# Kernel optimization log

Measured on AMD Instinct MI355X. Metric: run time of the kernel, lower is better.

The kernel has to match this reference:

```python
import jax, jax.numpy as jnp
import numpy as np

B, T, D = 2, 2048, 512
HEADS, DIM_HEAD, MAX_LAG = 8, 64, 5
INNER = HEADS * DIM_HEAD


def setup_inputs() -> dict:
    key = jax.random.key(0)
    k0, k1, k2, k3, k4 = jax.random.split(key, 5)
    x = jax.random.normal(k0, (B, T, D), dtype=jnp.float32)
    # Linear weights stored as (in, out); torch applies x @ W.T with W (out, in).
    Wq = jax.random.normal(k1, (D, INNER), dtype=jnp.float32) * (1.0 / np.sqrt(D))
    Wk = jax.random.normal(k2, (D, INNER), dtype=jnp.float32) * (1.0 / np.sqrt(D))
    Wv = jax.random.normal(k3, (D, INNER), dtype=jnp.float32) * (1.0 / np.sqrt(D))
    Wo = jax.random.normal(k4, (INNER, D), dtype=jnp.float32) * (1.0 / np.sqrt(INNER))
    bo = jnp.zeros((D,), dtype=jnp.float32)
    # Module's init: lag_weights = log(exp(-lags/(max_lag/3))) = -lags/(max_lag/3)
    lags = jnp.arange(MAX_LAG + 1, dtype=jnp.float32)
    lag_weights = jnp.broadcast_to(-(lags / (MAX_LAG / 3.0)), (HEADS, MAX_LAG + 1)).astype(jnp.float32)
    return {"x": x, "Wq": Wq, "Wk": Wk, "Wv": Wv, "Wo": Wo, "bo": bo, "lag_weights": lag_weights}


def reference(x, Wq, Wk, Wv, Wo, bo, lag_weights):
    b, t, _ = x.shape
    h, dh = HEADS, DIM_HEAD
    scale = dh ** -0.5
    # context defaults to x (self-attention)
    q = (x @ Wq).reshape(b, t, h, dh).transpose(0, 2, 1, 3)  # b h t d
    k = (x @ Wk).reshape(b, t, h, dh).transpose(0, 2, 1, 3)
    v = (x @ Wv).reshape(b, t, h, dh).transpose(0, 2, 1, 3)
    sim = jnp.einsum('bhid,bhjd->bhij', q, k) * scale  # b h t t
    # causal mask: keep j <= i
    causal = jnp.tril(jnp.ones((t, t), dtype=bool))
    neg = -jnp.finfo(sim.dtype).max
    sim = jnp.where(causal[None, None], sim, neg)
    # learned additive time-lag bias: lag_adj[h,i,j] = softmax(lag_weights)[h, clamp(i-j,0,MAX_LAG)]
    ti = jnp.arange(t)
    time_lags = jnp.clip(ti[:, None] - ti[None, :], 0, MAX_LAG)  # t t
    lag_probs = jax.nn.softmax(lag_weights, axis=-1)  # h (L+1)
    lag_adj = lag_probs[:, time_lags]  # h t t
    sim = sim + lag_adj[None]
    attn = jax.nn.softmax(sim, axis=-1)
    out = jnp.einsum('bhij,bhjd->bhid', attn, v)
    out = out.transpose(0, 2, 1, 3).reshape(b, t, h * dh)  # b t inner
    return out @ Wo + bo  # dropout is identity at eval
```

## Files before the change

kernel.cpp:

```cpp
#include <hip/hip_runtime.h>
#include <hip/hip_bf16.h>

#define BB 2
#define TT 2048
#define DD 512
#define HH 8
#define DH 64
#define INNER 512
#define MAXLAG 5

typedef __attribute__((ext_vector_type(8))) short short8;
typedef __attribute__((ext_vector_type(4))) float floatx4;
typedef unsigned short ushort_t;

__device__ inline unsigned short f2bf(float f) {
    unsigned u = __float_as_uint(f);
    unsigned r = (u + 0x7FFFu + ((u >> 16) & 1u)) >> 16;
    return (unsigned short)r;
}
__device__ inline float bf2f(unsigned short u) {
    return __uint_as_float(((unsigned)u) << 16);
}

__device__ __forceinline__ void gload16(ushort_t* lds, const ushort_t* g) {
    __builtin_amdgcn_global_load_lds(
        (const __attribute__((address_space(1))) void*)g,
        (__attribute__((address_space(3))) void*)lds, 16, 0, 0);
}

__global__ __launch_bounds__(256)
void cvt_kernel(const float* __restrict__ x,
                const float* __restrict__ wq, const float* __restrict__ wk,
                const float* __restrict__ wv, const float* __restrict__ wo,
                ushort_t* __restrict__ xb,
                ushort_t* __restrict__ wqkvt, ushort_t* __restrict__ wot)
{
    __shared__ float T[32][33];
    const int bid = blockIdx.x;
    if (bid < 1024) {
        int off = (bid * 256 + threadIdx.x) * 8;
        float4 a = *(const float4*)&x[off];
        float4 b = *(const float4*)&x[off + 4];
        ushort_t t[8];
        t[0] = f2bf(a.x); t[1] = f2bf(a.y); t[2] = f2bf(a.z); t[3] = f2bf(a.w);
        t[4] = f2bf(b.x); t[5] = f2bf(b.y); t[6] = f2bf(b.z); t[7] = f2bf(b.w);
        *(uint4*)&xb[off] = *(const uint4*)t;
        return;
    }
    const int r = bid - 1024;
    const int z = r >> 8;
    const int tile = r & 255;
    const float* s = (z == 0) ? wq : (z == 1) ? wk : (z == 2) ? wv : wo;
    ushort_t*    d = (z < 3) ? (wqkvt + (size_t)z * 512 * 512) : wot;
    const int k0 = (tile & 15) * 32;
    const int n0 = (tile >> 4) * 32;
    {
        const int kk = threadIdx.x >> 3;
        const int n4 = (threadIdx.x & 7) * 4;
        float4 v = *(const float4*)&s[(size_t)(k0 + kk) * 512 + n0 + n4];
        T[kk][n4 + 0] = v.x; T[kk][n4 + 1] = v.y;
        T[kk][n4 + 2] = v.z; T[kk][n4 + 3] = v.w;
    }
    __syncthreads();
    {
        const int nn = threadIdx.x >> 3;
        const int k4 = (threadIdx.x & 7) * 4;
        ushort4 o;
        o.x = f2bf(T[k4 + 0][nn]); o.y = f2bf(T[k4 + 1][nn]);
        o.z = f2bf(T[k4 + 2][nn]); o.w = f2bf(T[k4 + 3][nn]);
        *(ushort4*)&d[(size_t)(n0 + nn) * 512 + k0 + k4] = o;
    }
}

#define QM 128
#define QN 64
#define QKS 64

__global__ __launch_bounds__(256)
void gemm_qkv(const ushort_t* __restrict__ A, const ushort_t* __restrict__ Bw,
              ushort_t* __restrict__ q, ushort_t* __restrict__ k,
              ushort_t* __restrict__ vt)
{
    __shared__ ushort_t As[QM * QKS];
    __shared__ ushort_t Bs[QN * QKS];

    const int tid  = threadIdx.x;
    const int wave = tid >> 6;
    const int lane = tid & 63;
    const int quad = lane >> 4;
    const int l15  = lane & 15;
    const int wr   = wave >> 1;
    const int wc   = wave & 1;
    const int bm   = blockIdx.y * QM;
    const int bn   = blockIdx.x * QN;

    const int lr = lane >> 3;
    const int lc = lane & 7;

    const ushort_t* ap[4];
#pragma unroll
    for (int j = 0; j < 4; ++j) {
        const int row = wave * 32 + j * 8 + lr;
        const int c   = (lc - row) & 7;
        ap[j] = &A[(size_t)(bm + row) * DD + c * 8];
    }
    const ushort_t* bp[2];
#pragma unroll
    for (int j = 0; j < 2; ++j) {
        const int row = wave * 16 + j * 8 + lr;
        const int c   = (lc - row) & 7;
        bp[j] = &Bw[(size_t)(bn + row) * DD + c * 8];
    }
    ushort_t* lA0 = &As[(size_t)(wave * 256 +   0) * 8];
    ushort_t* lA1 = &As[(size_t)(wave * 256 +  64) * 8];
    ushort_t* lA2 = &As[(size_t)(wave * 256 + 128) * 8];
    ushort_t* lA3 = &As[(size_t)(wave * 256 + 192) * 8];
    ushort_t* lB0 = &Bs[(size_t)(wave * 128 +  0) * 8];
    ushort_t* lB1 = &Bs[(size_t)(wave * 128 + 64) * 8];

    floatx4 acc[4][2];
#pragma unroll
    for (int i = 0; i < 4; ++i)
#pragma unroll
        for (int j = 0; j < 2; ++j) acc[i][j] = (floatx4){0.f, 0.f, 0.f, 0.f};

#pragma unroll
    for (int k0 = 0; k0 < DD; k0 += QKS) {
        __syncthreads();
        gload16(lA0, ap[0] + k0);
        gload16(lA1, ap[1] + k0);
        gload16(lA2, ap[2] + k0);
        gload16(lA3, ap[3] + k0);
        gload16(lB0, bp[0] + k0);
        gload16(lB1, bp[1] + k0);
        __syncthreads();

#pragma unroll
        for (int kk = 0; kk < 2; ++kk) {
            short8 af[4], bfr[2];
#pragma unroll
            for (int mt = 0; mt < 4; ++mt) {
                const int row = wr * 64 + mt * 16 + l15;
                af[mt] = *(const short8*)
                    &As[((row << 3) + ((kk * 4 + quad + row) & 7)) * 8];
            }
#pragma unroll
            for (int nt = 0; nt < 2; ++nt) {
                const int row = wc * 32 + nt * 16 + l15;
                bfr[nt] = *(const short8*)
                    &Bs[((row << 3) + ((kk * 4 + quad + row) & 7)) * 8];
            }
#pragma unroll
            for (int mt = 0; mt < 4; ++mt)
#pragma unroll
                for (int nt = 0; nt < 2; ++nt)
                    acc[mt][nt] = __builtin_amdgcn_mfma_f32_16x16x32_bf16(
                        af[mt], bfr[nt], acc[mt][nt], 0, 0, 0);
        }
    }

    const int z = bn >> 9;
    if (z == 2) {
#pragma unroll
        for (int mt = 0; mt < 4; ++mt) {
            const int m0 = bm + wr * 64 + mt * 16 + quad * 4;
            const int b  = m0 >> 11;
            const int t0 = m0 & 2047;
#pragma unroll
            for (int nt = 0; nt < 2; ++nt) {
                const int n  = bn + wc * 32 + nt * 16 + l15 - 1024;
                const int h  = n >> 6, dd = n & 63;
                ushort4 o;
                o.x = f2bf(acc[mt][nt][0]); o.y = f2bf(acc[mt][nt][1]);
                o.z = f2bf(acc[mt][nt][2]); o.w = f2bf(acc[mt][nt][3]);
                *(ushort4*)&vt[((size_t)((b * 8 + h) * 64 + dd)) * 2048 + t0] = o;
            }
        }
        return;
    }
    ushort_t* O = (z == 0) ? q : k;
    const int nb = bn - z * 512;
#pragma unroll
    for (int mt = 0; mt < 4; ++mt) {
#pragma unroll
        for (int nt = 0; nt < 2; ++nt) {
            const int n = nb + wc * 32 + nt * 16 + l15;
#pragma unroll
            for (int reg = 0; reg < 4; ++reg) {
                const int m = bm + wr * 64 + mt * 16 + quad * 4 + reg;
                O[(size_t)m * 512 + n] = f2bf(acc[mt][nt][reg]);
            }
        }
    }
}

__global__ __launch_bounds__(256)
void gemm_proj(const ushort_t* __restrict__ A, const ushort_t* __restrict__ Bw,
               float* __restrict__ O, const float* __restrict__ bias)
{
    __shared__ ushort_t As[64 * 64];
    __shared__ ushort_t Bs[64 * 64];

    const int tid  = threadIdx.x;
    const int wave = tid >> 6;
    const int lane = tid & 63;
    const int quad = lane >> 4;
    const int l15  = lane & 15;
    const int wr   = wave >> 1;
    const int wc   = wave & 1;
    const int bm   = blockIdx.y * 64;
    const int bn   = blockIdx.x * 64;

    const int lr = lane >> 3;
    const int lc = lane & 7;

    const ushort_t* ap[2];
    const ushort_t* bp[2];
#pragma unroll
    for (int j = 0; j < 2; ++j) {
        const int row = wave * 16 + j * 8 + lr;
        const int c   = (lc - row) & 7;
        ap[j] = &A[(size_t)(bm + row) * INNER + c * 8];
        bp[j] = &Bw[(size_t)(bn + row) * INNER + c * 8];
    }
    ushort_t* lA0 = &As[(size_t)(wave * 128 +  0) * 8];
    ushort_t* lA1 = &As[(size_t)(wave * 128 + 64) * 8];
    ushort_t* lB0 = &Bs[(size_t)(wave * 128 +  0) * 8];
    ushort_t* lB1 = &Bs[(size_t)(wave * 128 + 64) * 8];

    floatx4 acc[2][2];
#pragma unroll
    for (int i = 0; i < 2; ++i)
#pragma unroll
        for (int j = 0; j < 2; ++j) acc[i][j] = (floatx4){0.f, 0.f, 0.f, 0.f};

#pragma unroll
    for (int k0 = 0; k0 < INNER; k0 += 64) {
        __syncthreads();
        gload16(lA0, ap[0] + k0);
        gload16(lA1, ap[1] + k0);
        gload16(lB0, bp[0] + k0);
        gload16(lB1, bp[1] + k0);
        __syncthreads();

#pragma unroll
        for (int kk = 0; kk < 2; ++kk) {
            short8 af[2], bfr[2];
#pragma unroll
            for (int mt = 0; mt < 2; ++mt) {
                const int row = wr * 32 + mt * 16 + l15;
                af[mt] = *(const short8*)
                    &As[((row << 3) + ((kk * 4 + quad + row) & 7)) * 8];
            }
#pragma unroll
            for (int nt = 0; nt < 2; ++nt) {
                const int row = wc * 32 + nt * 16 + l15;
                bfr[nt] = *(const short8*)
                    &Bs[((row << 3) + ((kk * 4 + quad + row) & 7)) * 8];
            }
#pragma unroll
            for (int mt = 0; mt < 2; ++mt)
#pragma unroll
                for (int nt = 0; nt < 2; ++nt)
                    acc[mt][nt] = __builtin_amdgcn_mfma_f32_16x16x32_bf16(
                        af[mt], bfr[nt], acc[mt][nt], 0, 0, 0);
        }
    }

    float bv[2];
#pragma unroll
    for (int nt = 0; nt < 2; ++nt)
        bv[nt] = bias[bn + wc * 32 + nt * 16 + l15];
#pragma unroll
    for (int mt = 0; mt < 2; ++mt) {
#pragma unroll
        for (int nt = 0; nt < 2; ++nt) {
            const int n = bn + wc * 32 + nt * 16 + l15;
#pragma unroll
            for (int reg = 0; reg < 4; ++reg) {
                const int m = bm + wr * 32 + mt * 16 + quad * 4 + reg;
                O[(size_t)m * 512 + n] = acc[mt][nt][reg] + bv[nt];
            }
        }
    }
}

#define PAD 72
#define MFIX 10.0f

__global__ __launch_bounds__(256)
void attn_mfma(const ushort_t* __restrict__ Qg,
               const ushort_t* __restrict__ Kg,
               const ushort_t* __restrict__ Vtg,
               const float* __restrict__ lagw,
               ushort_t* __restrict__ Opart,
               float* __restrict__ Lpart,
               ushort_t* __restrict__ ao)
{
    __shared__ ushort_t Ks[64 * 8 * 8];
    __shared__ ushort_t Vts[64 * 8 * 8];
    __shared__ ushort_t Pl[4][16][PAD];

    const int tid  = threadIdx.x;
    const int wave = tid >> 6;
    const int lane = tid & 63;
    const int quad = lane >> 4;
    const int l15  = lane & 15;

    const int f  = blockIdx.x;
    const int rr = f >> 4;
    const int bh = f & 15;
    int qt, ci;
    if (rr < 32)      { qt = 31 - (rr >> 2); ci = rr & 3; }
    else if (rr < 56) { const int t = rr - 32; qt = 23 - t / 3; ci = t % 3; }
    else if (rr < 72) { const int t = rr - 56; qt = 15 - (t >> 1); ci = t & 1; }
    else              { qt = 79 - rr; ci = 0; }
    const int lo = ci * 8;
    const int hi = min(lo + 8, qt + 1);
    const int nch = (qt >> 3) + 1;

    const int b  = bh >> 3;
    const int h  = bh & 7;
    const int i0 = qt * 64;

    float lagb[MAXLAG + 1];
    {
        float mx = -1e30f;
#pragma unroll
        for (int l = 0; l <= MAXLAG; ++l) {
            lagb[l] = lagw[h * (MAXLAG + 1) + l];
            mx = fmaxf(mx, lagb[l]);
        }
        float s = 0.f;
#pragma unroll
        for (int l = 0; l <= MAXLAG; ++l) { lagb[l] = __expf(lagb[l] - mx); s += lagb[l]; }
        float inv = 1.f / s;
#pragma unroll
        for (int l = 0; l <= MAXLAG; ++l) lagb[l] = lagb[l] * inv - MFIX;
    }
    const float c1  = 0.125f;
    const float c2f = lagb[MAXLAG];

    short8 qf0, qf1;
    {
        const ushort_t* qbase =
            Qg + ((size_t)(b * TT + i0 + wave * 16 + l15)) * INNER + h * DH;
        qf0 = *(const short8*)(qbase + quad * 8);
        qf1 = *(const short8*)(qbase + 32 + quad * 8);
    }

    floatx4 oacc[4];
    float lsum[4] = {0.f, 0.f, 0.f, 0.f};
#pragma unroll
    for (int cb = 0; cb < 4; ++cb) oacc[cb] = (floatx4){0.f, 0.f, 0.f, 0.f};

    const int ibase = i0 + wave * 16 + quad * 4;

    const int srow = tid >> 3;
    const int sc   = tid & 7;
    const ushort_t* Kp0 = Kg + ((size_t)(b * TT) + srow) * INNER + h * DH + sc * 8;
    const ushort_t* Kp1 = Kp0 + (size_t)32 * INNER;
    const ushort_t* Vp0 = Vtg + ((size_t)(bh * 64 + srow)) * 2048 + sc * 8;
    const ushort_t* Vp1 = Vp0 + (size_t)32 * 2048;
    const int slot = (sc + srow) & 7;
    const int kdst0 = ((srow << 3) + slot) << 3;
    const int kdst1 = (((srow + 32) << 3) + slot) << 3;

    uint4 pk0, pk1, pv0, pv1;
    {
        const size_t koff = (size_t)(lo * 64) * INNER;
        pk0 = *(const uint4*)(Kp0 + koff);
        pk1 = *(const uint4*)(Kp1 + koff);
        pv0 = *(const uint4*)(Vp0 + lo * 64);
        pv1 = *(const uint4*)(Vp1 + lo * 64);
    }

    for (int kt = lo; kt < hi; ++kt) {
        __syncthreads();
        *(uint4*)&Ks[kdst0]  = pk0;
        *(uint4*)&Ks[kdst1]  = pk1;
        *(uint4*)&Vts[kdst0] = pv0;
        *(uint4*)&Vts[kdst1] = pv1;
        __syncthreads();

        if (kt + 1 < hi) {
            const size_t koff = (size_t)((kt + 1) * 64) * INNER;
            pk0 = *(const uint4*)(Kp0 + koff);
            pk1 = *(const uint4*)(Kp1 + koff);
            pv0 = *(const uint4*)(Vp0 + (kt + 1) * 64);
            pv1 = *(const uint4*)(Vp1 + (kt + 1) * 64);
        }

        const int j0 = kt * 64;

        floatx4 sacc[4];
#pragma unroll
        for (int cb = 0; cb < 4; ++cb) {
            const int key = cb * 16 + l15;
            short8 kf0 = *(const short8*)&Ks[((key << 3) + ((quad + key) & 7)) << 3];
            short8 kf1 = *(const short8*)&Ks[((key << 3) + ((quad + 4 + key) & 7)) << 3];
            floatx4 zf = (floatx4){0.f, 0.f, 0.f, 0.f};
            zf = __builtin_amdgcn_mfma_f32_16x16x32_bf16(qf0, kf0, zf, 0, 0, 0);
            zf = __builtin_amdgcn_mfma_f32_16x16x32_bf16(qf1, kf1, zf, 0, 0, 0);
            sacc[cb] = zf;
        }

        float p[4][4];
        if (i0 + wave * 16 - (j0 + 63) >= MAXLAG) {
#pragma unroll
            for (int cb = 0; cb < 4; ++cb)
#pragma unroll
                for (int reg = 0; reg < 4; ++reg)
                    p[cb][reg] = __expf(fmaf(sacc[cb][reg], c1, c2f));
        } else {
#pragma unroll
            for (int cb = 0; cb < 4; ++cb) {
                const int j = j0 + cb * 16 + l15;
#pragma unroll
                for (int reg = 0; reg < 4; ++reg) {
                    const int lag = (ibase + reg) - j;
                    float bias = (lag <= 0) ? lagb[0]
                               : (lag == 1) ? lagb[1]
                               : (lag == 2) ? lagb[2]
                               : (lag == 3) ? lagb[3]
                               : (lag == 4) ? lagb[4] : lagb[5];
                    float e = __expf(fmaf(sacc[cb][reg], c1, bias));
                    p[cb][reg] = (lag < 0) ? 0.f : e;
                }
            }
        }
#pragma unroll
        for (int cb = 0; cb < 4; ++cb)
#pragma unroll
            for (int reg = 0; reg < 4; ++reg)
                lsum[reg] += p[cb][reg];

#pragma unroll
        for (int cb = 0; cb < 4; ++cb)
#pragma unroll
            for (int reg = 0; reg < 4; ++reg)
                Pl[wave][quad * 4 + reg][cb * 16 + l15] = f2bf(p[cb][reg]);

        short8 pf0 = *(const short8*)&Pl[wave][l15][quad * 8];
        short8 pf1 = *(const short8*)&Pl[wave][l15][32 + quad * 8];

#pragma unroll
        for (int cb = 0; cb < 4; ++cb) {
            const int dd = cb * 16 + l15;
            short8 vf0 = *(const short8*)&Vts[((dd << 3) + ((quad + dd) & 7)) << 3];
            short8 vf1 = *(const short8*)&Vts[((dd << 3) + ((quad + 4 + dd) & 7)) << 3];
            oacc[cb] = __builtin_amdgcn_mfma_f32_16x16x32_bf16(pf0, vf0, oacc[cb], 0, 0, 0);
            oacc[cb] = __builtin_amdgcn_mfma_f32_16x16x32_bf16(pf1, vf1, oacc[cb], 0, 0, 0);
        }
    }

#pragma unroll
    for (int reg = 0; reg < 4; ++reg) {
        lsum[reg] += __shfl_xor(lsum[reg], 1);
        lsum[reg] += __shfl_xor(lsum[reg], 2);
        lsum[reg] += __shfl_xor(lsum[reg], 4);
        lsum[reg] += __shfl_xor(lsum[reg], 8);
    }

    if (nch == 1) {
#pragma unroll
        for (int reg = 0; reg < 4; ++reg) {
            const int row = ibase + reg;
            const float inv = 1.f / lsum[reg];
            ushort_t* dst = &ao[((size_t)(b * TT + row)) * INNER + h * DH];
#pragma unroll
            for (int cb = 0; cb < 4; ++cb)
                dst[cb * 16 + l15] = f2bf(oacc[cb][reg] * inv);
        }
        return;
    }

#pragma unroll
    for (int reg = 0; reg < 4; ++reg) {
        const int row = ibase + reg;
        const size_t obase = ((size_t)(ci * 16 + bh) * TT + row) * 64;
#pragma unroll
        for (int cb = 0; cb < 4; ++cb)
            Opart[obase + cb * 16 + l15] = f2bf(oacc[cb][reg]);
        if (l15 == 0)
            Lpart[(size_t)(ci * 16 + bh) * TT + row] = lsum[reg];
    }
}

#define CMB_ROWS (TT - 512)
#define CMB_UNITS (16 * CMB_ROWS * 16)

__global__ __launch_bounds__(256)
void combine_kernel(const ushort_t* __restrict__ Opart,
                    const float* __restrict__ Lpart,
                    ushort_t* __restrict__ ao)
{
    int u = blockIdx.x * 256 + threadIdx.x;
    const int bh  = u / (CMB_ROWS * 16);
    const int rem = u - bh * (CMB_ROWS * 16);
    const int i   = 512 + (rem >> 4);
    const int d   = (rem & 15) * 4;
    const int b   = bh >> 3;
    const int h   = bh & 7;
    const int nch = ((i >> 6) >> 3) + 1;

    float s0 = 0.f, s1 = 0.f, s2 = 0.f, s3 = 0.f, l = 0.f;
    for (int ci = 0; ci < nch; ++ci) {
        const size_t p = ((size_t)(ci * 16 + bh) * TT + i) * 64 + d;
        ushort4 a = *(const ushort4*)&Opart[p];
        s0 += bf2f(a.x); s1 += bf2f(a.y); s2 += bf2f(a.z); s3 += bf2f(a.w);
        l  += Lpart[(size_t)(ci * 16 + bh) * TT + i];
    }
    const float inv = 1.f / l;
    ushort4 o;
    o.x = f2bf(s0 * inv);
    o.y = f2bf(s1 * inv);
    o.z = f2bf(s2 * inv);
    o.w = f2bf(s3 * inv);
    *(ushort4*)&ao[((size_t)(b * TT + i)) * INNER + h * DH + d] = o;
}

extern "C" void kernel_launch(void* const* d_in, const int* in_sizes, int n_in,
                              void* d_out, int out_size, void* d_ws, size_t ws_size,
                              hipStream_t stream)
{
    const float* x  = (const float*)d_in[0];
    const float* Wq = (const float*)d_in[1];
    const float* Wk = (const float*)d_in[2];
    const float* Wv = (const float*)d_in[3];
    const float* Wo = (const float*)d_in[4];
    const float* bo = (const float*)d_in[5];
    const float* lw = (const float*)d_in[6];
    float* out = (float*)d_out;

    const size_t SZ  = (size_t)BB * TT * INNER;
    const size_t NWE = (size_t)DD * INNER;
    ushort_t* xb    = (ushort_t*)d_ws;
    ushort_t* wqkvt = xb + SZ;
    ushort_t* wot   = wqkvt + 3 * NWE;
    ushort_t* q     = wot + NWE;
    ushort_t* k     = q + SZ;
    ushort_t* vt    = k + SZ;
    ushort_t* opart = vt + SZ;
    float*    lpart = (float*)(opart + 4 * (size_t)16 * TT * 64);
    ushort_t* ao    = xb;

    cvt_kernel<<<2048, 256, 0, stream>>>(x, Wq, Wk, Wv, Wo, xb, wqkvt, wot);

    dim3 gQKV(3 * INNER / QN, (BB * TT) / QM);
    gemm_qkv<<<gQKV, 256, 0, stream>>>(xb, wqkvt, q, k, vt);

    attn_mfma<<<1280, 256, 0, stream>>>(q, k, vt, lw, opart, lpart, ao);

    combine_kernel<<<CMB_UNITS / 256, 256, 0, stream>>>(opart, lpart, ao);

    dim3 gPRJ(DD / 64, (BB * TT) / 64);
    gemm_proj<<<gPRJ, 256, 0, stream>>>(ao, wot, out, bo);
}
```

Baseline: 126.0 us.

## Process two 64-row query tiles per attention block to share K/V tiles

Each attention block now covers 128 query rows as two 64-row sub-tiles that reuse the same K and V tiles staged in shared memory. This halves global K/V traffic and the staging/barrier overhead per query row, and the grid shrinks from 1280 to 640 blocks. The split-K chunk schedule and the combine kernel's chunk count are recomputed for 128-row super-tiles. In exchange, the first sub-tile wastes work on the fully masked diagonal key tile, register pressure roughly doubles for accumulators, and fewer blocks are available to fill the CUs.

Result: slower. 133.1 us (+5.6%).

```diff
diff --git a/kernel.cpp b/kernel.cpp
--- a/kernel.cpp
+++ b/kernel.cpp
@@ -299,7 +299,8 @@
 {
     __shared__ ushort_t Ks[64 * 8 * 8];
     __shared__ ushort_t Vts[64 * 8 * 8];
-    __shared__ ushort_t Pl[4][16][PAD];
+    __shared__ ushort_t PlA[4][16][PAD];
+    __shared__ ushort_t PlB[4][16][PAD];
 
     const int tid  = threadIdx.x;
     const int wave = tid >> 6;
@@ -310,18 +311,18 @@
     const int f  = blockIdx.x;
     const int rr = f >> 4;
     const int bh = f & 15;
-    int qt, ci;
-    if (rr < 32)      { qt = 31 - (rr >> 2); ci = rr & 3; }
-    else if (rr < 56) { const int t = rr - 32; qt = 23 - t / 3; ci = t % 3; }
-    else if (rr < 72) { const int t = rr - 56; qt = 15 - (t >> 1); ci = t & 1; }
-    else              { qt = 79 - rr; ci = 0; }
-    const int lo = ci * 8;
-    const int hi = min(lo + 8, qt + 1);
-    const int nch = (qt >> 3) + 1;
+    int st, ci;
+    if (rr < 16)      { st = 15 - (rr >> 2); ci = rr & 3; }
+    else if (rr < 28) { const int t = rr - 16; st = 11 - t / 3; ci = t % 3; }
+    else if (rr < 36) { const int t = rr - 28; st = 7 - (t >> 1); ci = t & 1; }
+    else              { st = 39 - rr; ci = 0; }
+    const int lo  = ci * 8;
+    const int hi  = min(lo + 8, 2 * st + 2);
+    const int nch = (2 * st + 9) >> 3;
 
     const int b  = bh >> 3;
     const int h  = bh & 7;
-    const int i0 = qt * 64;
+    const int i0 = st * 128;
 
     float lagb[MAXLAG + 1];
     {
@@ -341,20 +342,28 @@
     const float c1  = 0.125f;
     const float c2f = lagb[MAXLAG];
 
-    short8 qf0, qf1;
+    short8 qf0a, qf1a, qf0b, qf1b;
     {
-        const ushort_t* qbase =
+        const ushort_t* qbaseA =
             Qg + ((size_t)(b * TT + i0 + wave * 16 + l15)) * INNER + h * DH;
-        qf0 = *(const short8*)(qbase + quad * 8);
-        qf1 = *(const short8*)(qbase + 32 + quad * 8);
-    }
-
-    floatx4 oacc[4];
-    float lsum[4] = {0.f, 0.f, 0.f, 0.f};
-#pragma unroll
-    for (int cb = 0; cb < 4; ++cb) oacc[cb] = (floatx4){0.f, 0.f, 0.f, 0.f};
-
-    const int ibase = i0 + wave * 16 + quad * 4;
+        const ushort_t* qbaseB = qbaseA + (size_t)64 * INNER;
+        qf0a = *(const short8*)(qbaseA + quad * 8);
+        qf1a = *(const short8*)(qbaseA + 32 + quad * 8);
+        qf0b = *(const short8*)(qbaseB + quad * 8);
+        qf1b = *(const short8*)(qbaseB + 32 + quad * 8);
+    }
+
+    floatx4 oaccA[4], oaccB[4];
+    float lsumA[4] = {0.f, 0.f, 0.f, 0.f};
+    float lsumB[4] = {0.f, 0.f, 0.f, 0.f};
+#pragma unroll
+    for (int cb = 0; cb < 4; ++cb) {
+        oaccA[cb] = (floatx4){0.f, 0.f, 0.f, 0.f};
+        oaccB[cb] = (floatx4){0.f, 0.f, 0.f, 0.f};
+    }
+
+    const int ibaseA = i0 + wave * 16 + quad * 4;
+    const int ibaseB = ibaseA + 64;
 
     const int srow = tid >> 3;
     const int sc   = tid & 7;
@@ -393,97 +402,149 @@
 
         const int j0 = kt * 64;
 
-        floatx4 sacc[4];
+        floatx4 saccA[4], saccB[4];
 #pragma unroll
         for (int cb = 0; cb < 4; ++cb) {
             const int key = cb * 16 + l15;
             short8 kf0 = *(const short8*)&Ks[((key << 3) + ((quad + key) & 7)) << 3];
             short8 kf1 = *(const short8*)&Ks[((key << 3) + ((quad + 4 + key) & 7)) << 3];
-            floatx4 zf = (floatx4){0.f, 0.f, 0.f, 0.f};
-            zf = __builtin_amdgcn_mfma_f32_16x16x32_bf16(qf0, kf0, zf, 0, 0, 0);
-            zf = __builtin_amdgcn_mfma_f32_16x16x32_bf16(qf1, kf1, zf, 0, 0, 0);
-            sacc[cb] = zf;
-        }
-
-        float p[4][4];
+            floatx4 za = (floatx4){0.f, 0.f, 0.f, 0.f};
+            za = __builtin_amdgcn_mfma_f32_16x16x32_bf16(qf0a, kf0, za, 0, 0, 0);
+            za = __builtin_amdgcn_mfma_f32_16x16x32_bf16(qf1a, kf1, za, 0, 0, 0);
+            saccA[cb] = za;
+            floatx4 zb = (floatx4){0.f, 0.f, 0.f, 0.f};
+            zb = __builtin_amdgcn_mfma_f32_16x16x32_bf16(qf0b, kf0, zb, 0, 0, 0);
+            zb = __builtin_amdgcn_mfma_f32_16x16x32_bf16(qf1b, kf1, zb, 0, 0, 0);
+            saccB[cb] = zb;
+        }
+
+        float pA[4][4];
         if (i0 + wave * 16 - (j0 + 63) >= MAXLAG) {
 #pragma unroll
             for (int cb = 0; cb < 4; ++cb)
 #pragma unroll
                 for (int reg = 0; reg < 4; ++reg)
-                    p[cb][reg] = __expf(fmaf(sacc[cb][reg], c1, c2f));
+                    pA[cb][reg] = __expf(fmaf(saccA[cb][reg], c1, c2f));
         } else {
 #pragma unroll
             for (int cb = 0; cb < 4; ++cb) {
                 const int j = j0 + cb * 16 + l15;
 #pragma unroll
                 for (int reg = 0; reg < 4; ++reg) {
-                    const int lag = (ibase + reg) - j;
+                    const int lag = (ibaseA + reg) - j;
                     float bias = (lag <= 0) ? lagb[0]
                                : (lag == 1) ? lagb[1]
                                : (lag == 2) ? lagb[2]
                                : (lag == 3) ? lagb[3]
                                : (lag == 4) ? lagb[4] : lagb[5];
-                    float e = __expf(fmaf(sacc[cb][reg], c1, bias));
-                    p[cb][reg] = (lag < 0) ? 0.f : e;
+                    float e = __expf(fmaf(saccA[cb][reg], c1, bias));
+                    pA[cb][reg] = (lag < 0) ? 0.f : e;
                 }
             }
         }
+        float pB[4][4];
+        if (i0 + 64 + wave * 16 - (j0 + 63) >= MAXLAG) {
+#pragma unroll
+            for (int cb = 0; cb < 4; ++cb)
+#pragma unroll
+                for (int reg = 0; reg < 4; ++reg)
+                    pB[cb][reg] = __expf(fmaf(saccB[cb][reg], c1, c2f));
+        } else {
+#pragma unroll
+            for (int cb = 0; cb < 4; ++cb) {
+                const int j = j0 + cb * 16 + l15;
+#pragma unroll
+                for (int reg = 0; reg < 4; ++reg) {
+                    const int lag = (ibaseB + reg) - j;
+                    float bias = (lag <= 0) ? lagb[0]
+                               : (lag == 1) ? lagb[1]
+                               : (lag == 2) ? lagb[2]
+                               : (lag == 3) ? lagb[3]
+                               : (lag == 4) ? lagb[4] : lagb[5];
+                    float e = __expf(fmaf(saccB[cb][reg], c1, bias));
+                    pB[cb][reg] = (lag < 0) ? 0.f : e;
+                }
+            }
+        }
+
 #pragma unroll
         for (int cb = 0; cb < 4; ++cb)
 #pragma unroll
-            for (int reg = 0; reg < 4; ++reg)
-                lsum[reg] += p[cb][reg];
+            for (int reg = 0; reg < 4; ++reg) {
+                lsumA[reg] += pA[cb][reg];
+                lsumB[reg] += pB[cb][reg];
+            }
 
 #pragma unroll
         for (int cb = 0; cb < 4; ++cb)
 #pragma unroll
-            for (int reg = 0; reg < 4; ++reg)
-                Pl[wave][quad * 4 + reg][cb * 16 + l15] = f2bf(p[cb][reg]);
-
-        short8 pf0 = *(const short8*)&Pl[wave][l15][quad * 8];
-        short8 pf1 = *(const short8*)&Pl[wave][l15][32 + quad * 8];
+            for (int reg = 0; reg < 4; ++reg) {
+                PlA[wave][quad * 4 + reg][cb * 16 + l15] = f2bf(pA[cb][reg]);
+                PlB[wave][quad * 4 + reg][cb * 16 + l15] = f2bf(pB[cb][reg]);
+            }
+
+        short8 pf0a = *(const short8*)&PlA[wave][l15][quad * 8];
+        short8 pf1a = *(const short8*)&PlA[wave][l15][32 + quad * 8];
+        short8 pf0b = *(const short8*)&PlB[wave][l15][quad * 8];
+        short8 pf1b = *(const short8*)&PlB[wave][l15][32 + quad * 8];
 
 #pragma unroll
         for (int cb = 0; cb < 4; ++cb) {
             const int dd = cb * 16 + l15;
             short8 vf0 = *(const short8*)&Vts[((dd << 3) + ((quad + dd) & 7)) << 3];
             short8 vf1 = *(const short8*)&Vts[((dd << 3) + ((quad + 4 + dd) & 7)) << 3];
-            oacc[cb] = __builtin_amdgcn_mfma_f32_16x16x32_bf16(pf0, vf0, oacc[cb], 0, 0, 0);
-            oacc[cb] = __builtin_amdgcn_mfma_f32_16x16x32_bf16(pf1, vf1, oacc[cb], 0, 0, 0);
+            oaccA[cb] = __builtin_amdgcn_mfma_f32_16x16x32_bf16(pf0a, vf0, oaccA[cb], 0, 0, 0);
+            oaccA[cb] = __builtin_amdgcn_mfma_f32_16x16x32_bf16(pf1a, vf1, oaccA[cb], 0, 0, 0);
+            oaccB[cb] = __builtin_amdgcn_mfma_f32_16x16x32_bf16(pf0b, vf0, oaccB[cb], 0, 0, 0);
+            oaccB[cb] = __builtin_amdgcn_mfma_f32_16x16x32_bf16(pf1b, vf1, oaccB[cb], 0, 0, 0);
         }
     }
 
 #pragma unroll
     for (int reg = 0; reg < 4; ++reg) {
-        lsum[reg] += __shfl_xor(lsum[reg], 1);
-        lsum[reg] += __shfl_xor(lsum[reg], 2);
-        lsum[reg] += __shfl_xor(lsum[reg], 4);
-        lsum[reg] += __shfl_xor(lsum[reg], 8);
+        lsumA[reg] += __shfl_xor(lsumA[reg], 1);
+        lsumA[reg] += __shfl_xor(lsumA[reg], 2);
+        lsumA[reg] += __shfl_xor(lsumA[reg], 4);
+        lsumA[reg] += __shfl_xor(lsumA[reg], 8);
+        lsumB[reg] += __shfl_xor(lsumB[reg], 1);
+        lsumB[reg] += __shfl_xor(lsumB[reg], 2);
+        lsumB[reg] += __shfl_xor(lsumB[reg], 4);
+        lsumB[reg] += __shfl_xor(lsumB[reg], 8);
     }
 
     if (nch == 1) {
 #pragma unroll
         for (int reg = 0; reg < 4; ++reg) {
-            const int row = ibase + reg;
-            const float inv = 1.f / lsum[reg];
-            ushort_t* dst = &ao[((size_t)(b * TT + row)) * INNER + h * DH];
-#pragma unroll
-            for (int cb = 0; cb < 4; ++cb)
-                dst[cb * 16 + l15] = f2bf(oacc[cb][reg] * inv);
+            const int rowA = ibaseA + reg;
+            const int rowB = ibaseB + reg;
+            const float invA = 1.f / lsumA[reg];
+            const float invB = 1.f / lsumB[reg];
+            ushort_t* dstA = &ao[((size_t)(b * TT + rowA)) * INNER + h * DH];
+            ushort_t* dstB = &ao[((size_t)(b * TT + rowB)) * INNER + h * DH];
+#pragma unroll
+            for (int cb = 0; cb < 4; ++cb) {
+                dstA[cb * 16 + l15] = f2bf(oaccA[cb][reg] * invA);
+                dstB[cb * 16 + l15] = f2bf(oaccB[cb][reg] * invB);
+            }
         }
         return;
     }
 
 #pragma unroll
     for (int reg = 0; reg < 4; ++reg) {
-        const int row = ibase + reg;
-        const size_t obase = ((size_t)(ci * 16 + bh) * TT + row) * 64;
-#pragma unroll
-        for (int cb = 0; cb < 4; ++cb)
-            Opart[obase + cb * 16 + l15] = f2bf(oacc[cb][reg]);
-        if (l15 == 0)
-            Lpart[(size_t)(ci * 16 + bh) * TT + row] = lsum[reg];
+        const int rowA = ibaseA + reg;
+        const int rowB = ibaseB + reg;
+        const size_t obA = ((size_t)(ci * 16 + bh) * TT + rowA) * 64;
+        const size_t obB = ((size_t)(ci * 16 + bh) * TT + rowB) * 64;
+#pragma unroll
+        for (int cb = 0; cb < 4; ++cb) {
+            Opart[obA + cb * 16 + l15] = f2bf(oaccA[cb][reg]);
+            Opart[obB + cb * 16 + l15] = f2bf(oaccB[cb][reg]);
+        }
+        if (l15 == 0) {
+            Lpart[(size_t)(ci * 16 + bh) * TT + rowA] = lsumA[reg];
+            Lpart[(size_t)(ci * 16 + bh) * TT + rowB] = lsumB[reg];
+        }
     }
 }
 
@@ -502,7 +563,7 @@
     const int d   = (rem & 15) * 4;
     const int b   = bh >> 3;
     const int h   = bh & 7;
-    const int nch = ((i >> 6) >> 3) + 1;
+    const int nch = (2 * (i >> 7) + 9) >> 3;
 
     float s0 = 0.f, s1 = 0.f, s2 = 0.f, s3 = 0.f, l = 0.f;
     for (int ci = 0; ci < nch; ++ci) {
@@ -550,7 +611,7 @@
     dim3 gQKV(3 * INNER / QN, (BB * TT) / QM);
     gemm_qkv<<<gQKV, 256, 0, stream>>>(xb, wqkvt, q, k, vt);
 
-    attn_mfma<<<1280, 256, 0, stream>>>(q, k, vt, lw, opart, lpart, ao);
+    attn_mfma<<<640, 256, 0, stream>>>(q, k, vt, lw, opart, lpart, ao);
 
     combine_kernel<<<CMB_UNITS / 256, 256, 0, stream>>>(opart, lpart, ao);
 
```
